# Performance work log

Hardware: AMD Instinct MI355X
Metric: run time of the kernel (lower is better)

The kernel has to match this reference:

```python
import jax, jax.numpy as jnp
import numpy as np

N_HEAD = 16
N_EMBD = 1024
HEAD_DIM = N_EMBD // N_HEAD


def setup_inputs() -> dict:
    key = jax.random.key(0)
    k1, k2, k3 = jax.random.split(key, 3)
    B, T, C = 2, 2048, N_EMBD
    x = jax.random.normal(k1, (B, T, C), dtype=jnp.float32)
    # Linear weights stored as (in, out); torch nn.Linear weight is (out,in), y = x @ W.T.
    # We store the already-transposed form so reference does x @ w.
    w_attn = jax.random.normal(k2, (C, 3 * C), dtype=jnp.float32) * (1.0 / np.sqrt(C))
    w_proj = jax.random.normal(k3, (C, C), dtype=jnp.float32) * (1.0 / np.sqrt(C))
    return {"x": x, "w_attn": w_attn, "w_proj": w_proj}


def reference(x, w_attn, w_proj):
    B, T, C = x.shape
    qkv = x @ w_attn                          # [B,T,3C]
    q, k, v = jnp.split(qkv, 3, axis=2)
    # [B,T,C] -> [B,H,T,D]
    def heads(t):
        return t.reshape(B, T, N_HEAD, HEAD_DIM).transpose(0, 2, 1, 3)
    q, k, v = heads(q), heads(k), heads(v)
    scale = 1.0 / np.sqrt(HEAD_DIM)
    att = jnp.einsum('bhqd,bhkd->bhqk', q, k) * scale  # [B,H,T,T]
    causal = jnp.tril(jnp.ones((T, T), dtype=bool))
    att = jnp.where(causal, att, -jnp.inf)
    att = jax.nn.softmax(att, axis=-1)
    y = jnp.einsum('bhqk,bhkd->bhqd', att, v)          # [B,H,T,D]
    y = y.transpose(0, 2, 1, 3).reshape(B, T, C)
    return y @ w_proj
```

## Files before the change

kernel.cpp:

```cpp
#include <hip/hip_runtime.h>
#include <hip/hip_bf16.h>
#include <stdint.h>

typedef unsigned short u16;
typedef unsigned int u32;
typedef unsigned long long u64;
typedef float f32x4 __attribute__((ext_vector_type(4)));
typedef float f32x16 __attribute__((ext_vector_type(16)));
typedef short bf16x8 __attribute__((ext_vector_type(8)));
typedef u32 u32x4 __attribute__((ext_vector_type(4)));

#define MFMA(a, b, c) __builtin_amdgcn_mfma_f32_16x16x32_bf16((a), (b), (c), 0, 0, 0)
#define MFMA32(a, b, c) __builtin_amdgcn_mfma_f32_32x32x16_bf16((a), (b), (c), 0, 0, 0)

__device__ __forceinline__ void gll16(const void* g, void* lds) {
  __builtin_amdgcn_global_load_lds(
      (const __attribute__((address_space(1))) u32*)(uintptr_t)g,
      (__attribute__((address_space(3))) u32*)(uintptr_t)lds, 16, 0, 0);
}

__device__ __forceinline__ u16 f2b(float f) {
  union { __hip_bfloat16 h; u16 u; } cv;
  cv.h = __float2bfloat16(f);
  return cv.u;
}
__device__ __forceinline__ float b2f(u16 b) {
  union { u32 u; float f; } cv;
  cv.u = (u32)b << 16;
  return cv.f;
}
__device__ __forceinline__ u32 cvtpk(float lo, float hi) {
  u32 r;
  asm("v_cvt_pk_bf16_f32 %0, %1, %2" : "=v"(r) : "v"(lo), "v"(hi));
  return r;
}

__device__ __forceinline__ int sw(int r) { return ((r ^ (r >> 3)) & 7) << 4; }

__global__ __launch_bounds__(256) void k_cvt(const float* __restrict__ in,
                                             u16* __restrict__ out, int n4) {
  int i = blockIdx.x * 256 + threadIdx.x;
  if (i >= n4) return;
  const float4 v = reinterpret_cast<const float4*>(in)[i];
  u32 lo = (u32)f2b(v.x) | ((u32)f2b(v.y) << 16);
  u32 hi = (u32)f2b(v.z) | ((u32)f2b(v.w) << 16);
  reinterpret_cast<uint2*>(out)[i] = make_uint2(lo, hi);
}

__global__ __launch_bounds__(256) void k_trcvt(const float* __restrict__ in,
                                               u16* __restrict__ out, int R, int C) {
  __shared__ float tile[64][65];
  const int tid = threadIdx.x;
  const int r0 = blockIdx.y * 64, c0 = blockIdx.x * 64;
  const int tr = tid >> 4;
  const int tc4 = (tid & 15) * 4;
#pragma unroll
  for (int i = 0; i < 4; ++i) {
    const float4 v = *reinterpret_cast<const float4*>(
        &in[(size_t)(r0 + i * 16 + tr) * C + c0 + tc4]);
    tile[i * 16 + tr][tc4 + 0] = v.x;
    tile[i * 16 + tr][tc4 + 1] = v.y;
    tile[i * 16 + tr][tc4 + 2] = v.z;
    tile[i * 16 + tr][tc4 + 3] = v.w;
  }
  __syncthreads();
#pragma unroll
  for (int i = 0; i < 4; ++i) {
    const int c = i * 16 + tr;
    const int r4 = tc4;
    u32 lo = (u32)f2b(tile[r4 + 0][c]) | ((u32)f2b(tile[r4 + 1][c]) << 16);
    u32 hi = (u32)f2b(tile[r4 + 2][c]) | ((u32)f2b(tile[r4 + 3][c]) << 16);
    *reinterpret_cast<uint2*>(&out[(size_t)(c0 + c) * R + r0 + r4]) =
        make_uint2(lo, hi);
  }
}

template <int F32OUT>
__global__ __launch_bounds__(256) void k_gemm(const u16* __restrict__ A,
                                              const u16* __restrict__ Bt,
                                              void* __restrict__ Cout,
                                              int M, int N, int K) {
  __shared__ u16 As[128 * 32];
  __shared__ u16 Bs[128 * 32];
  const int tid = threadIdx.x;
  const int lane = tid & 63;
  const int w = tid >> 6;
  const int wm = w >> 1, wn = w & 1;
  const int l15 = lane & 15, lg = lane >> 4;
  const int brow = blockIdx.y * 128;
  const int bcol = blockIdx.x * 128;

  f32x4 acc[4][4] = {};

  const int r0 = tid >> 2;
  const int k8 = (tid & 3) * 8;
  const u16* Ag0 = A + (size_t)(brow + r0) * K + k8;
  const u16* Ag1 = A + (size_t)(brow + 64 + r0) * K + k8;
  const u16* Bg0 = Bt + (size_t)(bcol + r0) * K + k8;
  const u16* Bg1 = Bt + (size_t)(bcol + 64 + r0) * K + k8;
  u16* Asl0 = As + tid * 8;
  u16* Asl1 = As + 2048 + tid * 8;
  u16* Bsl0 = Bs + tid * 8;
  u16* Bsl1 = Bs + 2048 + tid * 8;

  for (int k0 = 0; k0 < K; k0 += 32) {
    gll16(Ag0 + k0, Asl0);
    gll16(Ag1 + k0, Asl1);
    gll16(Bg0 + k0, Bsl0);
    gll16(Bg1 + k0, Bsl1);
    __syncthreads();
    bf16x8 a[4], b[4];
#pragma unroll
    for (int m = 0; m < 4; ++m)
      a[m] = *(const bf16x8*)&As[(wm * 64 + m * 16 + l15) * 32 + lg * 8];
#pragma unroll
    for (int n = 0; n < 4; ++n)
      b[n] = *(const bf16x8*)&Bs[(wn * 64 + n * 16 + l15) * 32 + lg * 8];
#pragma unroll
    for (int m = 0; m < 4; ++m)
#pragma unroll
      for (int n = 0; n < 4; ++n)
        acc[m][n] = MFMA(a[m], b[n], acc[m][n]);
    __syncthreads();
  }

#pragma unroll
  for (int m = 0; m < 4; ++m) {
    const int row = brow + wm * 64 + m * 16 + lg * 4;
#pragma unroll
    for (int n = 0; n < 4; ++n) {
      const int col = bcol + wn * 64 + n * 16 + l15;
#pragma unroll
      for (int r = 0; r < 4; ++r) {
        const float v = acc[m][n][r];
        if (F32OUT)
          ((float*)Cout)[(size_t)(row + r) * N + col] = v;
        else
          ((u16*)Cout)[(size_t)(row + r) * N + col] = f2b(v);
      }
    }
  }
}

__global__ __launch_bounds__(512, 1) void k_gemm1(const u16* __restrict__ A,
                                                  const u16* __restrict__ Bt,
                                                  u16* __restrict__ C) {
  __shared__ u16 As[2][256 * 64];
  __shared__ u16 Bs[2][192 * 64];
  const int tid = threadIdx.x;
  const int lane = tid & 63;
  const int w = tid >> 6;
  const int wm = w >> 2, wn = w & 3;
  const int l15 = lane & 15, lg = lane >> 4;

  const int bid = blockIdx.x;
  const int lin = (bid & 7) * 32 + (bid >> 3);
  const int bm = lin >> 4, bn = lin & 15;
  const size_t brow = (size_t)bm * 256, bcol = (size_t)bn * 192;

  const int sr = tid >> 3;
  const int scb = (tid & 7) * 16;
  const int gcol = (scb ^ sw(sr)) >> 1;
  const u16* Ag[4];
#pragma unroll
  for (int i = 0; i < 4; ++i) Ag[i] = A + (brow + i * 64 + sr) * 1024 + gcol;
  const u16* Bg[3];
#pragma unroll
  for (int i = 0; i < 3; ++i) Bg[i] = Bt + (bcol + i * 64 + sr) * 1024 + gcol;

  f32x4 acc[8][3] = {};

#pragma unroll
  for (int i = 0; i < 4; ++i) gll16(Ag[i], (char*)As[0] + i * 8192 + tid * 16);
#pragma unroll
  for (int i = 0; i < 3; ++i) gll16(Bg[i], (char*)Bs[0] + i * 8192 + tid * 16);
  asm volatile("s_waitcnt vmcnt(0) lgkmcnt(0)" ::: "memory");
  __builtin_amdgcn_s_barrier();
  __builtin_amdgcn_sched_barrier(0);

  for (int kt = 0; kt < 16; ++kt) {
    const int cur = kt & 1;
    const char* as = (const char*)As[cur];
    const char* bs = (const char*)Bs[cur];
    char* asn = (char*)As[cur ^ 1];
    char* bsn = (char*)Bs[cur ^ 1];
    const bool more = (kt + 1 < 16);
    const int ko = (kt + 1) * 64;

    bf16x8 bfr[3][2];
#pragma unroll
    for (int n = 0; n < 3; ++n) {
      const int row = wn * 48 + n * 16 + l15;
#pragma unroll
      for (int kh = 0; kh < 2; ++kh)
        bfr[n][kh] = *(const bf16x8*)(bs + row * 128 +
                                      ((kh * 64 + lg * 16) ^ sw(row)));
    }
#define GPHASE(MB, STAGE_A, STAGE_B, LAST)                                    \
    {                                                                         \
      bf16x8 af[2][2];                                                        \
      _Pragma("unroll")                                                       \
      for (int mm = 0; mm < 2; ++mm) {                                        \
        const int row = wm * 128 + (MB + mm) * 16 + l15;                      \
        _Pragma("unroll")                                                     \
        for (int kh = 0; kh < 2; ++kh)                                        \
          af[mm][kh] = *(const bf16x8*)(as + row * 128 +                      \
                                        ((kh * 64 + lg * 16) ^ sw(row)));     \
      }                                                                       \
      if (STAGE_A && more) {                                                  \
        _Pragma("unroll")                                                     \
        for (int i = 0; i < 4; ++i)                                           \
          gll16(Ag[i] + ko, asn + i * 8192 + tid * 16);                       \
      }                                                                       \
      if (STAGE_B && more) {                                                  \
        _Pragma("unroll")                                                     \
        for (int i = 0; i < 3; ++i)                                           \
          gll16(Bg[i] + ko, bsn + i * 8192 + tid * 16);                       \
      }                                                                       \
      __builtin_amdgcn_s_setprio(1);                                          \
      _Pragma("unroll")                                                       \
      for (int mm = 0; mm < 2; ++mm)                                          \
        _Pragma("unroll")                                                     \
        for (int n = 0; n < 3; ++n) {                                         \
          acc[MB + mm][n] = MFMA(af[mm][0], bfr[n][0], acc[MB + mm][n]);      \
          acc[MB + mm][n] = MFMA(af[mm][1], bfr[n][1], acc[MB + mm][n]);      \
        }                                                                     \
      __builtin_amdgcn_s_setprio(0);                                          \
      if (LAST) {                                                             \
        asm volatile("s_waitcnt vmcnt(0) lgkmcnt(0)" ::: "memory");           \
      }                                                                       \
      __builtin_amdgcn_s_barrier();                                           \
    }
    GPHASE(0, 1, 0, 0)
    GPHASE(2, 0, 1, 0)
    GPHASE(4, 0, 0, 0)
    GPHASE(6, 0, 0, 1)
#undef GPHASE
    __builtin_amdgcn_sched_barrier(0);
  }

#pragma unroll
  for (int m = 0; m < 8; ++m) {
    const size_t row = brow + wm * 128 + m * 16 + lg * 4;
#pragma unroll
    for (int n = 0; n < 3; ++n) {
      const size_t col = bcol + wn * 48 + n * 16 + l15;
#pragma unroll
      for (int r = 0; r < 4; ++r)
        C[(row + r) * 3072 + col] = f2b(acc[m][n][r]);
    }
  }
}

__global__ __launch_bounds__(512, 1) void k_attn(const u16* __restrict__ qkv,
                                                 u16* __restrict__ y) {
  __shared__ u16 Kl[3][64 * 64];
  __shared__ u16 Vt[2][64 * 64];
  __shared__ float Om[4][64][33];
  __shared__ float Lm[4][2][32];
  const int tid = threadIdx.x;
  const int lane = tid & 63;
  const int w = tid >> 6;
  const int qsub = w & 3, tsub = w >> 2;
  const int l31 = lane & 31, hi = lane >> 5;

  const int lin = blockIdx.x;
  const int xcd = lin & 7;
  const int idx = lin >> 3;
  const int bh = xcd * 4 + (idx >> 3);
  const int pidx = idx & 7;
  const int b = bh >> 4, h = bh & 15;

  const u16* Qg = qkv + (size_t)(b * 2048) * 3072 + h * 64;
  const u16* Kg = Qg + 1024;
  const u16* Vg = Qg + 2048;

  const int srow = tid >> 3;
  const int scol = (((tid & 7) * 16) ^ sw(srow)) >> 1;
  const bool vstage = (tid < 256);
  const int t2 = (tid & 255) >> 3;
  const int d8 = (tid & 7) * 8;

  bf16x8 vone;
#pragma unroll
  for (int j = 0; j < 8; ++j) vone[j] = (short)0x3F80;

  const int trow = tsub * 32 + l31;
  int koff[4];
#pragma unroll
  for (int ks = 0; ks < 4; ++ks)
    koff[ks] = trow * 128 + (((ks * 16 + hi * 8) * 2) ^ sw(trow));
  int voff[2][2];
#pragma unroll
  for (int db = 0; db < 2; ++db) {
    const int dl = db * 32 + l31;
#pragma unroll
    for (int ks = 0; ks < 2; ++ks)
      voff[db][ks] = dl * 128 + (((tsub * 32 + ks * 16 + hi * 8) * 2) ^ sw(dl));
  }

  for (int pass = 0; pass < 2; ++pass) {
    const int qi = pass ? (15 - pidx) : pidx;
    const int nt = 2 * (qi + 1);
    const int qb = qi * 128;
    const int qrow = qb + qsub * 32 + l31;

    bf16x8 aq[4];
#pragma unroll
    for (int ks = 0; ks < 4; ++ks) {
      bf16x8 v = *(const bf16x8*)&Qg[(size_t)qrow * 3072 + ks * 16 + hi * 8];
#pragma unroll
      for (int j = 0; j < 8; ++j)
        v[j] = (short)f2b(b2f((u16)v[j]) * 0.18033688011112042f);
      aq[ks] = v;
    }

    f32x16 acc0 = {}, acc1 = {}, accl = {};

    bf16x8 va0, va1;
    {
      bf16x8 v00, v01;
      if (vstage) {
        v00 = *(const bf16x8*)&Vg[(size_t)(2 * t2) * 3072 + d8];
        v01 = *(const bf16x8*)&Vg[(size_t)(2 * t2 + 1) * 3072 + d8];
        va0 = *(const bf16x8*)&Vg[(size_t)(64 + 2 * t2) * 3072 + d8];
        va1 = *(const bf16x8*)&Vg[(size_t)(64 + 2 * t2 + 1) * 3072 + d8];
      }
      gll16(Kg + (size_t)srow * 3072 + scol, (u16*)Kl[0] + tid * 8);
      gll16(Kg + (size_t)(64 + srow) * 3072 + scol, (u16*)Kl[1] + tid * 8);
      if (vstage) {
#pragma unroll
        for (int j = 0; j < 8; ++j) {
          const int d = d8 + j;
          const u32 val = (u32)(u16)v00[j] | ((u32)(u16)v01[j] << 16);
          *(u32*)((char*)Vt[0] + ((d * 128 + t2 * 4) ^ sw(d))) = val;
        }
      }
    }
    asm volatile("s_waitcnt vmcnt(1) lgkmcnt(0)" ::: "memory");
    __builtin_amdgcn_s_barrier();
    __builtin_amdgcn_sched_barrier(0);

    const char* kR = (const char*)Kl[0];
    const char* kN = (const char*)Kl[1];
    char* kN2 = (char*)Kl[2];
    const char* vR = (const char*)Vt[0];
    char* vW = (char*)Vt[1];

    for (int t = 0; t < nt; ++t) {
      const int tf = (t + 2 < 31 ? t + 2 : 31);
      bf16x8 vf0, vf1;
      if (vstage) {
        vf0 = *(const bf16x8*)&Vg[(size_t)(tf * 64 + 2 * t2) * 3072 + d8];
        vf1 = *(const bf16x8*)&Vg[(size_t)(tf * 64 + 2 * t2 + 1) * 3072 + d8];
      }
      gll16(Kg + (size_t)(tf * 64 + srow) * 3072 + scol, (u16*)kN2 + tid * 8);

      f32x16 s = {};
#pragma unroll
      for (int ks = 0; ks < 4; ++ks) {
        const bf16x8 kf = *(const bf16x8*)(kR + koff[ks]);
        s = MFMA32(kf, aq[ks], s);
      }

      float p[16];
      if (t >= nt - 2) {
#pragma unroll
        for (int r = 0; r < 16; ++r) {
          const int kkg = t * 64 + tsub * 32 + (r & 3) + 8 * (r >> 2) + 4 * hi;
          p[r] = exp2f(kkg > qrow ? -1e30f : s[r]);
        }
      } else {
#pragma unroll
        for (int r = 0; r < 16; ++r) p[r] = exp2f(s[r]);
      }

      const u32 X0 = cvtpk(p[0], p[1]),   X1 = cvtpk(p[2], p[3]);
      const u32 X2 = cvtpk(p[4], p[5]),   X3 = cvtpk(p[6], p[7]);
      const u32 X4 = cvtpk(p[8], p[9]),   X5 = cvtpk(p[10], p[11]);
      const u32 X6 = cvtpk(p[12], p[13]), X7 = cvtpk(p[14], p[15]);
      const u32 sx0 = (u32)__shfl_xor((int)X0, 32);
      const u32 sx1 = (u32)__shfl_xor((int)X1, 32);
      const u32 sx2 = (u32)__shfl_xor((int)X2, 32);
      const u32 sx3 = (u32)__shfl_xor((int)X3, 32);
      const u32 sx4 = (u32)__shfl_xor((int)X4, 32);
      const u32 sx5 = (u32)__shfl_xor((int)X5, 32);
      const u32 sx6 = (u32)__shfl_xor((int)X6, 32);
      const u32 sx7 = (u32)__shfl_xor((int)X7, 32);
      union { u32x4 u; bf16x8 h; } c0, c1;
      c0.u[0] = hi ? sx2 : X0;
      c0.u[1] = hi ? sx3 : X1;
      c0.u[2] = hi ? X2 : sx0;
      c0.u[3] = hi ? X3 : sx1;
      c1.u[0] = hi ? sx6 : X4;
      c1.u[1] = hi ? sx7 : X5;
      c1.u[2] = hi ? X6 : sx4;
      c1.u[3] = hi ? X7 : sx5;
      const bf16x8 pb0 = c0.h, pb1 = c1.h;

      accl = MFMA32(vone, pb0, accl);
      accl = MFMA32(vone, pb1, accl);
      const bf16x8 vb00 = *(const bf16x8*)(vR + voff[0][0]);
      const bf16x8 vb01 = *(const bf16x8*)(vR + voff[0][1]);
      const bf16x8 vb10 = *(const bf16x8*)(vR + voff[1][0]);
      const bf16x8 vb11 = *(const bf16x8*)(vR + voff[1][1]);
      acc0 = MFMA32(vb00, pb0, acc0);
      acc0 = MFMA32(vb01, pb1, acc0);
      acc1 = MFMA32(vb10, pb0, acc1);
      acc1 = MFMA32(vb11, pb1, acc1);

      if (vstage && t < nt - 1) {
#pragma unroll
        for (int j = 0; j < 8; ++j) {
          const int d = d8 + j;
          const u32 val = (u32)(u16)va0[j] | ((u32)(u16)va1[j] << 16);
          *(u32*)(vW + ((d * 128 + t2 * 4) ^ sw(d))) = val;
        }
      }
      va0 = vf0; va1 = vf1;
      const char* kt = kR; kR = kN; kN = kN2; kN2 = (char*)kt;
      char* vt_ = (char*)vR; vR = vW; vW = vt_;

      asm volatile("s_waitcnt vmcnt(1) lgkmcnt(0)" ::: "memory");
      __builtin_amdgcn_s_barrier();
      __builtin_amdgcn_sched_barrier(0);
    }

    asm volatile("s_waitcnt vmcnt(0) lgkmcnt(0)" ::: "memory");
    __builtin_amdgcn_s_barrier();
    __builtin_amdgcn_sched_barrier(0);

    if (tsub == 1) {
#pragma unroll
      for (int r = 0; r < 16; ++r) {
        const int d = (r & 3) + 8 * (r >> 2) + 4 * hi;
        Om[qsub][d][l31] = acc0[r];
        Om[qsub][32 + d][l31] = acc1[r];
      }
      Lm[qsub][1][l31] = accl[0];
    } else {
      Lm[qsub][0][l31] = accl[0];
    }
    __syncthreads();
    if (tsub == 0) {
      const float linv = 1.0f / (Lm[qsub][0][l31] + Lm[qsub][1][l31]);
#pragma unroll
      for (int r = 0; r < 16; ++r) {
        const int d = (r & 3) + 8 * (r >> 2) + 4 * hi;
        Om[qsub][d][l31] = (acc0[r] + Om[qsub][d][l31]) * linv;
        Om[qsub][32 + d][l31] = (acc1[r] + Om[qsub][32 + d][l31]) * linv;
      }
    }
    __syncthreads();
    {
      const int qloc = tid >> 2;
      const int dgr = (tid & 3) * 16;
      const size_t yo = (size_t)(b * 2048 + qb + qloc) * 1024 + h * 64 + dgr;
      u32 o[8];
#pragma unroll
      for (int jj = 0; jj < 8; ++jj)
        o[jj] = cvtpk(Om[qloc >> 5][dgr + 2 * jj][qloc & 31],
                      Om[qloc >> 5][dgr + 2 * jj + 1][qloc & 31]);
      u32x4 s0 = {o[0], o[1], o[2], o[3]};
      u32x4 s1 = {o[4], o[5], o[6], o[7]};
      *(u32x4*)&y[yo] = s0;
      *(u32x4*)&y[yo + 8] = s1;
    }
    __syncthreads();
  }
}

extern "C" void kernel_launch(void* const* d_in, const int* in_sizes, int n_in,
                              void* d_out, int out_size, void* d_ws, size_t ws_size,
                              hipStream_t stream) {
  const float* x  = (const float*)d_in[0];
  const float* wa = (const float*)d_in[1];
  const float* wp = (const float*)d_in[2];
  float* out = (float*)d_out;

  u16* xb  = (u16*)d_ws;
  u16* wat = xb + (size_t)4096 * 1024;
  u16* wpt = wat + (size_t)3072 * 1024;
  u16* qkv = wpt + (size_t)1024 * 1024;
  u16* yb  = qkv + (size_t)4096 * 3072;

  k_cvt<<<4096, 256, 0, stream>>>(x, xb, 4096 * 1024 / 4);
  k_trcvt<<<dim3(3072 / 64, 1024 / 64), 256, 0, stream>>>(wa, wat, 1024, 3072);
  k_trcvt<<<dim3(1024 / 64, 1024 / 64), 256, 0, stream>>>(wp, wpt, 1024, 1024);

  k_gemm1<<<256, 512, 0, stream>>>(xb, wat, qkv);

  k_attn<<<256, 512, 0, stream>>>(qkv, yb);

  k_gemm<1><<<dim3(1024 / 128, 4096 / 128), 256, 0, stream>>>(yb, wpt, out, 4096, 1024, 1024);
}
```

Measured before the change: 119.0 us.

## Split attention blocks per query tile and alias shared memory for higher occupancy

The attention kernel now launches one block per (batch-head, query tile) instead of looping over two paired tiles inside a block, which doubles the grid to 512 blocks. Shared memory is packed into a single 40KB buffer, with the output reduction scratch aliased over the K/V staging area. The launch bound is raised to allow several blocks per CU. The aim is more resident waves to hide latency and better load balance across CUs, at the cost of losing the in-block pairing of short and long causal tiles and of tighter register limits.

```diff
diff --git a/kernel.cpp b/kernel.cpp
--- a/kernel.cpp
+++ b/kernel.cpp
@@ -252,23 +252,29 @@
   }
 }
 
-__global__ __launch_bounds__(512, 1) void k_attn(const u16* __restrict__ qkv,
+__global__ __launch_bounds__(512, 4) void k_attn(const u16* __restrict__ qkv,
                                                  u16* __restrict__ y) {
-  __shared__ u16 Kl[3][64 * 64];
-  __shared__ u16 Vt[2][64 * 64];
-  __shared__ float Om[4][64][33];
-  __shared__ float Lm[4][2][32];
+  __shared__ char smem[40960];
+  char* KlB = smem;
+  char* VtB = smem + 24576;
+  float (*Om)[64][33] = (float (*)[64][33])smem;
+  float (*Lm)[2][32] = (float (*)[2][32])(smem + 33792);
+
   const int tid = threadIdx.x;
   const int lane = tid & 63;
   const int w = tid >> 6;
   const int qsub = w & 3, tsub = w >> 2;
   const int l31 = lane & 31, hi = lane >> 5;
 
-  const int lin = blockIdx.x;
-  const int xcd = lin & 7;
-  const int idx = lin >> 3;
-  const int bh = xcd * 4 + (idx >> 3);
-  const int pidx = idx & 7;
+  const int bid = blockIdx.x;
+  const int xcd = bid & 7;
+  const int j = bid >> 3;
+  const int half = j >> 5;
+  const int jj = j & 31;
+  const int hl = half * 2 + (jj >> 4);
+  const int qi0 = jj & 15;
+  const int qi = half ? (15 - qi0) : qi0;
+  const int bh = xcd * 4 + hl;
   const int b = bh >> 4, h = bh & 15;
 
   const u16* Qg = qkv + (size_t)(b * 2048) * 3072 + h * 64;
@@ -283,7 +289,7 @@
 
   bf16x8 vone;
 #pragma unroll
-  for (int j = 0; j < 8; ++j) vone[j] = (short)0x3F80;
+  for (int jn = 0; jn < 8; ++jn) vone[jn] = (short)0x3F80;
 
   const int trow = tsub * 32 + l31;
   int koff[4];
@@ -299,174 +305,170 @@
       voff[db][ks] = dl * 128 + (((tsub * 32 + ks * 16 + hi * 8) * 2) ^ sw(dl));
   }
 
-  for (int pass = 0; pass < 2; ++pass) {
-    const int qi = pass ? (15 - pidx) : pidx;
-    const int nt = 2 * (qi + 1);
-    const int qb = qi * 128;
-    const int qrow = qb + qsub * 32 + l31;
-
-    bf16x8 aq[4];
+  const int nt = 2 * (qi + 1);
+  const int qb = qi * 128;
+  const int qrow = qb + qsub * 32 + l31;
+
+  bf16x8 aq[4];
+#pragma unroll
+  for (int ks = 0; ks < 4; ++ks) {
+    bf16x8 v = *(const bf16x8*)&Qg[(size_t)qrow * 3072 + ks * 16 + hi * 8];
+#pragma unroll
+    for (int jn = 0; jn < 8; ++jn)
+      v[jn] = (short)f2b(b2f((u16)v[jn]) * 0.18033688011112042f);
+    aq[ks] = v;
+  }
+
+  f32x16 acc0 = {}, acc1 = {}, accl = {};
+
+  bf16x8 va0, va1;
+  {
+    bf16x8 v00, v01;
+    if (vstage) {
+      v00 = *(const bf16x8*)&Vg[(size_t)(2 * t2) * 3072 + d8];
+      v01 = *(const bf16x8*)&Vg[(size_t)(2 * t2 + 1) * 3072 + d8];
+      va0 = *(const bf16x8*)&Vg[(size_t)(64 + 2 * t2) * 3072 + d8];
+      va1 = *(const bf16x8*)&Vg[(size_t)(64 + 2 * t2 + 1) * 3072 + d8];
+    }
+    gll16(Kg + (size_t)srow * 3072 + scol, (u16*)KlB + tid * 8);
+    gll16(Kg + (size_t)(64 + srow) * 3072 + scol, (u16*)(KlB + 8192) + tid * 8);
+    if (vstage) {
+#pragma unroll
+      for (int jn = 0; jn < 8; ++jn) {
+        const int d = d8 + jn;
+        const u32 val = (u32)(u16)v00[jn] | ((u32)(u16)v01[jn] << 16);
+        *(u32*)(VtB + ((d * 128 + t2 * 4) ^ sw(d))) = val;
+      }
+    }
+  }
+  asm volatile("s_waitcnt vmcnt(1) lgkmcnt(0)" ::: "memory");
+  __builtin_amdgcn_s_barrier();
+  __builtin_amdgcn_sched_barrier(0);
+
+  const char* kR = KlB;
+  const char* kN = KlB + 8192;
+  char* kN2 = KlB + 16384;
+  const char* vR = VtB;
+  char* vW = VtB + 8192;
+
+  for (int t = 0; t < nt; ++t) {
+    const int tf = (t + 2 < 31 ? t + 2 : 31);
+    bf16x8 vf0, vf1;
+    if (vstage) {
+      vf0 = *(const bf16x8*)&Vg[(size_t)(tf * 64 + 2 * t2) * 3072 + d8];
+      vf1 = *(const bf16x8*)&Vg[(size_t)(tf * 64 + 2 * t2 + 1) * 3072 + d8];
+    }
+    gll16(Kg + (size_t)(tf * 64 + srow) * 3072 + scol, (u16*)kN2 + tid * 8);
+
+    f32x16 s = {};
 #pragma unroll
     for (int ks = 0; ks < 4; ++ks) {
-      bf16x8 v = *(const bf16x8*)&Qg[(size_t)qrow * 3072 + ks * 16 + hi * 8];
-#pragma unroll
-      for (int j = 0; j < 8; ++j)
-        v[j] = (short)f2b(b2f((u16)v[j]) * 0.18033688011112042f);
-      aq[ks] = v;
-    }
-
-    f32x16 acc0 = {}, acc1 = {}, accl = {};
-
-    bf16x8 va0, va1;
-    {
-      bf16x8 v00, v01;
-      if (vstage) {
-        v00 = *(const bf16x8*)&Vg[(size_t)(2 * t2) * 3072 + d8];
-        v01 = *(const bf16x8*)&Vg[(size_t)(2 * t2 + 1) * 3072 + d8];
-        va0 = *(const bf16x8*)&Vg[(size_t)(64 + 2 * t2) * 3072 + d8];
-        va1 = *(const bf16x8*)&Vg[(size_t)(64 + 2 * t2 + 1) * 3072 + d8];
+      const bf16x8 kf = *(const bf16x8*)(kR + koff[ks]);
+      s = MFMA32(kf, aq[ks], s);
+    }
+
+    float p[16];
+    if (t >= nt - 2) {
+#pragma unroll
+      for (int r = 0; r < 16; ++r) {
+        const int kkg = t * 64 + tsub * 32 + (r & 3) + 8 * (r >> 2) + 4 * hi;
+        p[r] = exp2f(kkg > qrow ? -1e30f : s[r]);
       }
-      gll16(Kg + (size_t)srow * 3072 + scol, (u16*)Kl[0] + tid * 8);
-      gll16(Kg + (size_t)(64 + srow) * 3072 + scol, (u16*)Kl[1] + tid * 8);
-      if (vstage) {
-#pragma unroll
-        for (int j = 0; j < 8; ++j) {
-          const int d = d8 + j;
-          const u32 val = (u32)(u16)v00[j] | ((u32)(u16)v01[j] << 16);
-          *(u32*)((char*)Vt[0] + ((d * 128 + t2 * 4) ^ sw(d))) = val;
-        }
+    } else {
+#pragma unroll
+      for (int r = 0; r < 16; ++r) p[r] = exp2f(s[r]);
+    }
+
+    const u32 X0 = cvtpk(p[0], p[1]),   X1 = cvtpk(p[2], p[3]);
+    const u32 X2 = cvtpk(p[4], p[5]),   X3 = cvtpk(p[6], p[7]);
+    const u32 X4 = cvtpk(p[8], p[9]),   X5 = cvtpk(p[10], p[11]);
+    const u32 X6 = cvtpk(p[12], p[13]), X7 = cvtpk(p[14], p[15]);
+    const u32 sx0 = (u32)__shfl_xor((int)X0, 32);
+    const u32 sx1 = (u32)__shfl_xor((int)X1, 32);
+    const u32 sx2 = (u32)__shfl_xor((int)X2, 32);
+    const u32 sx3 = (u32)__shfl_xor((int)X3, 32);
+    const u32 sx4 = (u32)__shfl_xor((int)X4, 32);
+    const u32 sx5 = (u32)__shfl_xor((int)X5, 32);
+    const u32 sx6 = (u32)__shfl_xor((int)X6, 32);
+    const u32 sx7 = (u32)__shfl_xor((int)X7, 32);
+    union { u32x4 u; bf16x8 h; } c0, c1;
+    c0.u[0] = hi ? sx2 : X0;
+    c0.u[1] = hi ? sx3 : X1;
+    c0.u[2] = hi ? X2 : sx0;
+    c0.u[3] = hi ? X3 : sx1;
+    c1.u[0] = hi ? sx6 : X4;
+    c1.u[1] = hi ? sx7 : X5;
+    c1.u[2] = hi ? X6 : sx4;
+    c1.u[3] = hi ? X7 : sx5;
+    const bf16x8 pb0 = c0.h, pb1 = c1.h;
+
+    accl = MFMA32(vone, pb0, accl);
+    accl = MFMA32(vone, pb1, accl);
+    const bf16x8 vb00 = *(const bf16x8*)(vR + voff[0][0]);
+    const bf16x8 vb01 = *(const bf16x8*)(vR + voff[0][1]);
+    const bf16x8 vb10 = *(const bf16x8*)(vR + voff[1][0]);
+    const bf16x8 vb11 = *(const bf16x8*)(vR + voff[1][1]);
+    acc0 = MFMA32(vb00, pb0, acc0);
+    acc0 = MFMA32(vb01, pb1, acc0);
+    acc1 = MFMA32(vb10, pb0, acc1);
+    acc1 = MFMA32(vb11, pb1, acc1);
+
+    if (vstage && t < nt - 1) {
+#pragma unroll
+      for (int jn = 0; jn < 8; ++jn) {
+        const int d = d8 + jn;
+        const u32 val = (u32)(u16)va0[jn] | ((u32)(u16)va1[jn] << 16);
+        *(u32*)(vW + ((d * 128 + t2 * 4) ^ sw(d))) = val;
       }
     }
+    va0 = vf0; va1 = vf1;
+    const char* kt_ = kR; kR = kN; kN = kN2; kN2 = (char*)kt_;
+    char* vt_ = (char*)vR; vR = vW; vW = vt_;
+
     asm volatile("s_waitcnt vmcnt(1) lgkmcnt(0)" ::: "memory");
     __builtin_amdgcn_s_barrier();
     __builtin_amdgcn_sched_barrier(0);
-
-    const char* kR = (const char*)Kl[0];
-    const char* kN = (const char*)Kl[1];
-    char* kN2 = (char*)Kl[2];
-    const char* vR = (const char*)Vt[0];
-    char* vW = (char*)Vt[1];
-
-    for (int t = 0; t < nt; ++t) {
-      const int tf = (t + 2 < 31 ? t + 2 : 31);
-      bf16x8 vf0, vf1;
-      if (vstage) {
-        vf0 = *(const bf16x8*)&Vg[(size_t)(tf * 64 + 2 * t2) * 3072 + d8];
-        vf1 = *(const bf16x8*)&Vg[(size_t)(tf * 64 + 2 * t2 + 1) * 3072 + d8];
-      }
-      gll16(Kg + (size_t)(tf * 64 + srow) * 3072 + scol, (u16*)kN2 + tid * 8);
-
-      f32x16 s = {};
-#pragma unroll
-      for (int ks = 0; ks < 4; ++ks) {
-        const bf16x8 kf = *(const bf16x8*)(kR + koff[ks]);
-        s = MFMA32(kf, aq[ks], s);
-      }
-
-      float p[16];
-      if (t >= nt - 2) {
-#pragma unroll
-        for (int r = 0; r < 16; ++r) {
-          const int kkg = t * 64 + tsub * 32 + (r & 3) + 8 * (r >> 2) + 4 * hi;
-          p[r] = exp2f(kkg > qrow ? -1e30f : s[r]);
-        }
-      } else {
-#pragma unroll
-        for (int r = 0; r < 16; ++r) p[r] = exp2f(s[r]);
-      }
-
-      const u32 X0 = cvtpk(p[0], p[1]),   X1 = cvtpk(p[2], p[3]);
-      const u32 X2 = cvtpk(p[4], p[5]),   X3 = cvtpk(p[6], p[7]);
-      const u32 X4 = cvtpk(p[8], p[9]),   X5 = cvtpk(p[10], p[11]);
-      const u32 X6 = cvtpk(p[12], p[13]), X7 = cvtpk(p[14], p[15]);
-      const u32 sx0 = (u32)__shfl_xor((int)X0, 32);
-      const u32 sx1 = (u32)__shfl_xor((int)X1, 32);
-      const u32 sx2 = (u32)__shfl_xor((int)X2, 32);
-      const u32 sx3 = (u32)__shfl_xor((int)X3, 32);
-      const u32 sx4 = (u32)__shfl_xor((int)X4, 32);
-      const u32 sx5 = (u32)__shfl_xor((int)X5, 32);
-      const u32 sx6 = (u32)__shfl_xor((int)X6, 32);
-      const u32 sx7 = (u32)__shfl_xor((int)X7, 32);
-      union { u32x4 u; bf16x8 h; } c0, c1;
-      c0.u[0] = hi ? sx2 : X0;
-      c0.u[1] = hi ? sx3 : X1;
-      c0.u[2] = hi ? X2 : sx0;
-      c0.u[3] = hi ? X3 : sx1;
-      c1.u[0] = hi ? sx6 : X4;
-      c1.u[1] = hi ? sx7 : X5;
-      c1.u[2] = hi ? X6 : sx4;
-      c1.u[3] = hi ? X7 : sx5;
-      const bf16x8 pb0 = c0.h, pb1 = c1.h;
-
-      accl = MFMA32(vone, pb0, accl);
-      accl = MFMA32(vone, pb1, accl);
-      const bf16x8 vb00 = *(const bf16x8*)(vR + voff[0][0]);
-      const bf16x8 vb01 = *(const bf16x8*)(vR + voff[0][1]);
-      const bf16x8 vb10 = *(const bf16x8*)(vR + voff[1][0]);
-      const bf16x8 vb11 = *(const bf16x8*)(vR + voff[1][1]);
-      acc0 = MFMA32(vb00, pb0, acc0);
-      acc0 = MFMA32(vb01, pb1, acc0);
-      acc1 = MFMA32(vb10, pb0, acc1);
-      acc1 = MFMA32(vb11, pb1, acc1);
-
-      if (vstage && t < nt - 1) {
-#pragma unroll
-        for (int j = 0; j < 8; ++j) {
-          const int d = d8 + j;
-          const u32 val = (u32)(u16)va0[j] | ((u32)(u16)va1[j] << 16);
-          *(u32*)(vW + ((d * 128 + t2 * 4) ^ sw(d))) = val;
-        }
-      }
-      va0 = vf0; va1 = vf1;
-      const char* kt = kR; kR = kN; kN = kN2; kN2 = (char*)kt;
-      char* vt_ = (char*)vR; vR = vW; vW = vt_;
-
-      asm volatile("s_waitcnt vmcnt(1) lgkmcnt(0)" ::: "memory");
-      __builtin_amdgcn_s_barrier();
-      __builtin_amdgcn_sched_barrier(0);
-    }
-
-    asm volatile("s_waitcnt vmcnt(0) lgkmcnt(0)" ::: "memory");
-    __builtin_amdgcn_s_barrier();
-    __builtin_amdgcn_sched_barrier(0);
-
-    if (tsub == 1) {
-#pragma unroll
-      for (int r = 0; r < 16; ++r) {
-        const int d = (r & 3) + 8 * (r >> 2) + 4 * hi;
-        Om[qsub][d][l31] = acc0[r];
-        Om[qsub][32 + d][l31] = acc1[r];
-      }
-      Lm[qsub][1][l31] = accl[0];
-    } else {
-      Lm[qsub][0][l31] = accl[0];
-    }
-    __syncthreads();
-    if (tsub == 0) {
-      const float linv = 1.0f / (Lm[qsub][0][l31] + Lm[qsub][1][l31]);
-#pragma unroll
-      for (int r = 0; r < 16; ++r) {
-        const int d = (r & 3) + 8 * (r >> 2) + 4 * hi;
-        Om[qsub][d][l31] = (acc0[r] + Om[qsub][d][l31]) * linv;
-        Om[qsub][32 + d][l31] = (acc1[r] + Om[qsub][32 + d][l31]) * linv;
-      }
-    }
-    __syncthreads();
-    {
-      const int qloc = tid >> 2;
-      const int dgr = (tid & 3) * 16;
-      const size_t yo = (size_t)(b * 2048 + qb + qloc) * 1024 + h * 64 + dgr;
-      u32 o[8];
-#pragma unroll
-      for (int jj = 0; jj < 8; ++jj)
-        o[jj] = cvtpk(Om[qloc >> 5][dgr + 2 * jj][qloc & 31],
-                      Om[qloc >> 5][dgr + 2 * jj + 1][qloc & 31]);
-      u32x4 s0 = {o[0], o[1], o[2], o[3]};
-      u32x4 s1 = {o[4], o[5], o[6], o[7]};
-      *(u32x4*)&y[yo] = s0;
-      *(u32x4*)&y[yo + 8] = s1;
-    }
-    __syncthreads();
+  }
+
+  asm volatile("s_waitcnt vmcnt(0) lgkmcnt(0)" ::: "memory");
+  __builtin_amdgcn_s_barrier();
+  __builtin_amdgcn_sched_barrier(0);
+
+  if (tsub == 1) {
+#pragma unroll
+    for (int r = 0; r < 16; ++r) {
+      const int d = (r & 3) + 8 * (r >> 2) + 4 * hi;
+      Om[qsub][d][l31] = acc0[r];
+      Om[qsub][32 + d][l31] = acc1[r];
+    }
+    Lm[qsub][1][l31] = accl[0];
+  } else {
+    Lm[qsub][0][l31] = accl[0];
+  }
+  __syncthreads();
+  if (tsub == 0) {
+    const float linv = 1.0f / (Lm[qsub][0][l31] + Lm[qsub][1][l31]);
+#pragma unroll
+    for (int r = 0; r < 16; ++r) {
+      const int d = (r & 3) + 8 * (r >> 2) + 4 * hi;
+      Om[qsub][d][l31] = (acc0[r] + Om[qsub][d][l31]) * linv;
+      Om[qsub][32 + d][l31] = (acc1[r] + Om[qsub][32 + d][l31]) * linv;
+    }
+  }
+  __syncthreads();
+  {
+    const int qloc = tid >> 2;
+    const int dgr = (tid & 3) * 16;
+    const size_t yo = (size_t)(b * 2048 + qb + qloc) * 1024 + h * 64 + dgr;
+    u32 o[8];
+#pragma unroll
+    for (int jn = 0; jn < 8; ++jn)
+      o[jn] = cvtpk(Om[qloc >> 5][dgr + 2 * jn][qloc & 31],
+                    Om[qloc >> 5][dgr + 2 * jn + 1][qloc & 31]);
+    u32x4 s0 = {o[0], o[1], o[2], o[3]};
+    u32x4 s1 = {o[4], o[5], o[6], o[7]};
+    *(u32x4*)&y[yo] = s0;
+    *(u32x4*)&y[yo + 8] = s1;
   }
 }
 
@@ -490,7 +492,7 @@
 
   k_gemm1<<<256, 512, 0, stream>>>(xb, wat, qkv);
 
-  k_attn<<<256, 512, 0, stream>>>(qkv, yb);
+  k_attn<<<512, 512, 0, stream>>>(qkv, yb);
 
   k_gemm<1><<<dim3(1024 / 128, 4096 / 128), 256, 0, stream>>>(yb, wpt, out, 4096, 1024, 1024);
 }
```

Measured after the change: 161.4 us. +35.6%, slower.

## Replace generic projection GEMM with double-buffered swizzled pipelined kernel

Applied to the files above, without the earlier changes.

The output projection GEMM moves from a simple single-buffered kernel with K-step 32 to a dedicated kernel. The new kernel uses double-buffered LDS with K-step 64, XOR-swizzled LDS layout and global-to-LDS prefetch interleaved with MFMA phases. It also adds an XCD-aware block remap and setprio around the MFMAs. The aim is to hide global load latency and cut barrier overhead, at the cost of more LDS use and sizes hardcoded to 4096x1024x1024.

```diff
diff --git a/kernel.cpp b/kernel.cpp
--- a/kernel.cpp
+++ b/kernel.cpp
@@ -72,73 +72,6 @@
     u32 hi = (u32)f2b(tile[r4 + 2][c]) | ((u32)f2b(tile[r4 + 3][c]) << 16);
     *reinterpret_cast<uint2*>(&out[(size_t)(c0 + c) * R + r0 + r4]) =
         make_uint2(lo, hi);
-  }
-}
-
-template <int F32OUT>
-__global__ __launch_bounds__(256) void k_gemm(const u16* __restrict__ A,
-                                              const u16* __restrict__ Bt,
-                                              void* __restrict__ Cout,
-                                              int M, int N, int K) {
-  __shared__ u16 As[128 * 32];
-  __shared__ u16 Bs[128 * 32];
-  const int tid = threadIdx.x;
-  const int lane = tid & 63;
-  const int w = tid >> 6;
-  const int wm = w >> 1, wn = w & 1;
-  const int l15 = lane & 15, lg = lane >> 4;
-  const int brow = blockIdx.y * 128;
-  const int bcol = blockIdx.x * 128;
-
-  f32x4 acc[4][4] = {};
-
-  const int r0 = tid >> 2;
-  const int k8 = (tid & 3) * 8;
-  const u16* Ag0 = A + (size_t)(brow + r0) * K + k8;
-  const u16* Ag1 = A + (size_t)(brow + 64 + r0) * K + k8;
-  const u16* Bg0 = Bt + (size_t)(bcol + r0) * K + k8;
-  const u16* Bg1 = Bt + (size_t)(bcol + 64 + r0) * K + k8;
-  u16* Asl0 = As + tid * 8;
-  u16* Asl1 = As + 2048 + tid * 8;
-  u16* Bsl0 = Bs + tid * 8;
-  u16* Bsl1 = Bs + 2048 + tid * 8;
-
-  for (int k0 = 0; k0 < K; k0 += 32) {
-    gll16(Ag0 + k0, Asl0);
-    gll16(Ag1 + k0, Asl1);
-    gll16(Bg0 + k0, Bsl0);
-    gll16(Bg1 + k0, Bsl1);
-    __syncthreads();
-    bf16x8 a[4], b[4];
-#pragma unroll
-    for (int m = 0; m < 4; ++m)
-      a[m] = *(const bf16x8*)&As[(wm * 64 + m * 16 + l15) * 32 + lg * 8];
-#pragma unroll
-    for (int n = 0; n < 4; ++n)
-      b[n] = *(const bf16x8*)&Bs[(wn * 64 + n * 16 + l15) * 32 + lg * 8];
-#pragma unroll
-    for (int m = 0; m < 4; ++m)
-#pragma unroll
-      for (int n = 0; n < 4; ++n)
-        acc[m][n] = MFMA(a[m], b[n], acc[m][n]);
-    __syncthreads();
-  }
-
-#pragma unroll
-  for (int m = 0; m < 4; ++m) {
-    const int row = brow + wm * 64 + m * 16 + lg * 4;
-#pragma unroll
-    for (int n = 0; n < 4; ++n) {
-      const int col = bcol + wn * 64 + n * 16 + l15;
-#pragma unroll
-      for (int r = 0; r < 4; ++r) {
-        const float v = acc[m][n][r];
-        if (F32OUT)
-          ((float*)Cout)[(size_t)(row + r) * N + col] = v;
-        else
-          ((u16*)Cout)[(size_t)(row + r) * N + col] = f2b(v);
-      }
-    }
   }
 }
 
@@ -248,6 +181,115 @@
 #pragma unroll
       for (int r = 0; r < 4; ++r)
         C[(row + r) * 3072 + col] = f2b(acc[m][n][r]);
+    }
+  }
+}
+
+__global__ __launch_bounds__(256) void k_gemm2(const u16* __restrict__ A,
+                                               const u16* __restrict__ Bt,
+                                               float* __restrict__ C) {
+  __shared__ u16 As[2][128 * 64];
+  __shared__ u16 Bs[2][128 * 64];
+  const int tid = threadIdx.x;
+  const int lane = tid & 63;
+  const int w = tid >> 6;
+  const int wm = w >> 1, wn = w & 1;
+  const int l15 = lane & 15, lg = lane >> 4;
+
+  const int bid = blockIdx.x;
+  const int lin = (bid & 7) * 32 + (bid >> 3);
+  const int bm = lin >> 3, bn = lin & 7;
+  const size_t brow = (size_t)bm * 128, bcol = (size_t)bn * 128;
+
+  const int sr = tid >> 3;
+  const int scb = (tid & 7) * 16;
+  const u16* Ag[4];
+  const u16* Bg[4];
+#pragma unroll
+  for (int i = 0; i < 4; ++i) {
+    const int row = i * 32 + sr;
+    const int gcol = (scb ^ sw(row)) >> 1;
+    Ag[i] = A + (brow + row) * 1024 + gcol;
+    Bg[i] = Bt + (bcol + row) * 1024 + gcol;
+  }
+
+  f32x4 acc[4][4] = {};
+
+#pragma unroll
+  for (int i = 0; i < 4; ++i) gll16(Ag[i], (char*)As[0] + i * 4096 + tid * 16);
+#pragma unroll
+  for (int i = 0; i < 4; ++i) gll16(Bg[i], (char*)Bs[0] + i * 4096 + tid * 16);
+  asm volatile("s_waitcnt vmcnt(0) lgkmcnt(0)" ::: "memory");
+  __builtin_amdgcn_s_barrier();
+  __builtin_amdgcn_sched_barrier(0);
+
+  for (int kt = 0; kt < 16; ++kt) {
+    const int cur = kt & 1;
+    const char* as = (const char*)As[cur];
+    const char* bs = (const char*)Bs[cur];
+    char* asn = (char*)As[cur ^ 1];
+    char* bsn = (char*)Bs[cur ^ 1];
+    const bool more = (kt + 1 < 16);
+    const int ko = (kt + 1) * 64;
+
+    bf16x8 bfr[4][2];
+#pragma unroll
+    for (int n = 0; n < 4; ++n) {
+      const int row = wn * 64 + n * 16 + l15;
+#pragma unroll
+      for (int kh = 0; kh < 2; ++kh)
+        bfr[n][kh] = *(const bf16x8*)(bs + row * 128 +
+                                      ((kh * 64 + lg * 16) ^ sw(row)));
+    }
+#define G2PHASE(MB, STAGE_A, STAGE_B, LAST)                                   \
+    {                                                                         \
+      bf16x8 af[2];                                                           \
+      {                                                                       \
+        const int row = wm * 64 + (MB) * 16 + l15;                            \
+        _Pragma("unroll")                                                     \
+        for (int kh = 0; kh < 2; ++kh)                                        \
+          af[kh] = *(const bf16x8*)(as + row * 128 +                          \
+                                    ((kh * 64 + lg * 16) ^ sw(row)));         \
+      }                                                                       \
+      if (STAGE_A && more) {                                                  \
+        _Pragma("unroll")                                                     \
+        for (int i = 0; i < 4; ++i)                                           \
+          gll16(Ag[i] + ko, asn + i * 4096 + tid * 16);                       \
+      }                                                                       \
+      if (STAGE_B && more) {                                                  \
+        _Pragma("unroll")                                                     \
+        for (int i = 0; i < 4; ++i)                                           \
+          gll16(Bg[i] + ko, bsn + i * 4096 + tid * 16);                       \
+      }                                                                       \
+      __builtin_amdgcn_s_setprio(1);                                          \
+      _Pragma("unroll")                                                       \
+      for (int n = 0; n < 4; ++n) {                                           \
+        acc[MB][n] = MFMA(af[0], bfr[n][0], acc[MB][n]);                      \
+        acc[MB][n] = MFMA(af[1], bfr[n][1], acc[MB][n]);                      \
+      }                                                                       \
+      __builtin_amdgcn_s_setprio(0);                                          \
+      if (LAST) {                                                             \
+        asm volatile("s_waitcnt vmcnt(0) lgkmcnt(0)" ::: "memory");           \
+      }                                                                       \
+      __builtin_amdgcn_s_barrier();                                           \
+    }
+    G2PHASE(0, 1, 0, 0)
+    G2PHASE(1, 0, 1, 0)
+    G2PHASE(2, 0, 0, 0)
+    G2PHASE(3, 0, 0, 1)
+#undef G2PHASE
+    __builtin_amdgcn_sched_barrier(0);
+  }
+
+#pragma unroll
+  for (int m = 0; m < 4; ++m) {
+    const size_t row = brow + wm * 64 + m * 16 + lg * 4;
+#pragma unroll
+    for (int n = 0; n < 4; ++n) {
+      const size_t col = bcol + wn * 64 + n * 16 + l15;
+#pragma unroll
+      for (int r = 0; r < 4; ++r)
+        C[(row + r) * 1024 + col] = acc[m][n][r];
     }
   }
 }
@@ -492,5 +534,5 @@
 
   k_attn<<<256, 512, 0, stream>>>(qkv, yb);
 
-  k_gemm<1><<<dim3(1024 / 128, 4096 / 128), 256, 0, stream>>>(yb, wpt, out, 4096, 1024, 1024);
-}
+  k_gemm2<<<256, 256, 0, stream>>>(yb, wpt, out);
+}
```

Result: faster. 107.6 us (median of 2 runs) (-9.6%).
